# Kernel tuning notes

Measured on AMD Instinct MI355X. Metric: run time of the kernel, lower is better.

## Reference

```python
import jax, jax.numpy as jnp
import numpy as np

DIM = 384
HEADS = 6
HEAD_DIM = DIM // HEADS
MLP_DIM = int(DIM * 4.0)
EPS = 1e-5


def layer_norm(x, g, b):
    mu = jnp.mean(x, axis=-1, keepdims=True)
    var = jnp.mean(jnp.square(x - mu), axis=-1, keepdims=True)
    return (x - mu) * jax.lax.rsqrt(var + EPS) * g + b


def setup_inputs() -> dict:
    key = jax.random.key(0)
    ks = jax.random.split(key, 12)
    s = 0.02
    return {
        "x": jax.random.normal(ks[0], (8, 2048, DIM), dtype=jnp.float32),
        "ln1_g": jnp.ones((DIM,), jnp.float32),
        "ln1_b": jnp.zeros((DIM,), jnp.float32),
        "qkv_w": jax.random.normal(ks[1], (DIM, 3 * DIM), jnp.float32) * s,
        "qkv_b": jnp.zeros((3 * DIM,), jnp.float32),
        "proj_w": jax.random.normal(ks[2], (DIM, DIM), jnp.float32) * s,
        "proj_b": jnp.zeros((DIM,), jnp.float32),
        "ln2_g": jnp.ones((DIM,), jnp.float32),
        "ln2_b": jnp.zeros((DIM,), jnp.float32),
        "fc1_w": jax.random.normal(ks[3], (DIM, MLP_DIM), jnp.float32) * s,
        "fc1_b": jnp.zeros((MLP_DIM,), jnp.float32),
        "fc2_w": jax.random.normal(ks[4], (MLP_DIM, DIM), jnp.float32) * s,
        "fc2_b": jnp.zeros((DIM,), jnp.float32),
    }


def reference(x, ln1_g, ln1_b, qkv_w, qkv_b, proj_w, proj_b,
              ln2_g, ln2_b, fc1_w, fc1_b, fc2_w, fc2_b):
    B, N, C = x.shape
    # --- attention ---
    h = layer_norm(x, ln1_g, ln1_b)
    qkv = h @ qkv_w + qkv_b  # [B,N,3C]
    qkv = qkv.reshape(B, N, 3, HEADS, HEAD_DIM)
    q, k, v = jnp.moveaxis(qkv, 2, 0)  # each [B,N,H,D]
    scale = HEAD_DIM ** -0.5
    attn = jnp.einsum('bnhd,bmhd->bhnm', q, k) * scale  # [B,H,N,N]
    attn = jax.nn.softmax(attn, axis=-1)
    o = jnp.einsum('bhnm,bmhd->bnhd', attn, v).reshape(B, N, C)
    x = x + o @ proj_w + proj_b
    # --- mlp ---
    h = layer_norm(x, ln2_g, ln2_b)
    h = jax.nn.gelu(h @ fc1_w + fc1_b, approximate=False)
    x = x + h @ fc2_w + fc2_b
    return x
```

## Files before the change

kernel.cpp:

```cpp
#include <hip/hip_runtime.h>
#include <hip/hip_bf16.h>

#define DIM   384
#define SEQ   2048
#define BATCH 8
#define NHEAD 6
#define HD    64
#define MLPD  1536
#define MTOT  (BATCH*SEQ)

typedef __attribute__((ext_vector_type(8))) short bf16x8;
typedef __attribute__((ext_vector_type(4))) float f32x4;

static __device__ __forceinline__ float bf2f(unsigned short u){
    union { float f; unsigned int i; } v; v.i = ((unsigned int)u) << 16; return v.f;
}
static __device__ __forceinline__ unsigned short f2bf(float f){
    union { float f; unsigned int i; } v; v.f = f;
    unsigned int r = v.i + 0x7fffu + ((v.i >> 16) & 1u);
    return (unsigned short)(r >> 16);
}
static __device__ __forceinline__ unsigned int asu(float f){
    union { float f; unsigned int i; } v; v.f = f; return v.i;
}
static __device__ __forceinline__ void gload_lds16(const unsigned short* g, unsigned short* l){
    __builtin_amdgcn_global_load_lds(
        (__attribute__((address_space(1))) void*)(g),
        (__attribute__((address_space(3))) void*)(l), 16, 0, 0);
}
static __device__ __forceinline__ void barx(){
    asm volatile("" ::: "memory");
    __builtin_amdgcn_s_barrier();
    asm volatile("" ::: "memory");
}
#define WAITVM(N) asm volatile("s_waitcnt vmcnt(" #N ")" ::: "memory")

__global__ __launch_bounds__(256) void wt_all_kernel(
    const float* __restrict__ qkv_w, const float* __restrict__ proj_w,
    const float* __restrict__ fc1_w, const float* __restrict__ fc2_w,
    unsigned short* __restrict__ o_qkv, unsigned short* __restrict__ o_prj,
    unsigned short* __restrict__ o_fc1, unsigned short* __restrict__ o_fc2)
{
    __shared__ float tile[64][68];
    int bid = blockIdx.x;
    const float* W; unsigned short* Wt; int K, N, tk, tn;
    if (bid < 108)      { W = qkv_w; Wt = o_qkv; K = 384;  N = 1152; tk = bid/18;        tn = bid%18; }
    else if (bid < 144) { W = proj_w; Wt = o_prj; K = 384;  N = 384;  tk = (bid-108)/6;  tn = (bid-108)%6; }
    else if (bid < 288) { W = fc1_w; Wt = o_fc1; K = 384;  N = 1536; tk = (bid-144)/24; tn = (bid-144)%24; }
    else                { W = fc2_w; Wt = o_fc2; K = 1536; N = 384;  tk = (bid-288)/6;  tn = (bid-288)%6; }
    int t = threadIdx.x;
    int lr = t >> 4, lc = (t & 15) * 4;
#pragma unroll
    for (int p = 0; p < 4; p++){
        float4 v = *(const float4*)(W + (size_t)(tk*64 + p*16 + lr) * N + tn*64 + lc);
        *(float4*)&tile[p*16 + lr][lc] = v;
    }
    __syncthreads();
    int n = t >> 2, k0 = (t & 3) * 16;
    unsigned int w[8];
#pragma unroll
    for (int i = 0; i < 8; i++)
        w[i] = (unsigned int)f2bf(tile[k0 + 2*i][n]) | ((unsigned int)f2bf(tile[k0 + 2*i + 1][n]) << 16);
    unsigned short* dst = Wt + (size_t)(tn*64 + n) * K + tk*64 + k0;
    *(uint4*)(dst)     = make_uint4(w[0], w[1], w[2], w[3]);
    *(uint4*)(dst + 8) = make_uint4(w[4], w[5], w[6], w[7]);
}

__global__ __launch_bounds__(256) void ln_kernel(const float* __restrict__ x,
                                                 const float* __restrict__ g,
                                                 const float* __restrict__ b,
                                                 unsigned short* __restrict__ out){
    int row  = blockIdx.x * 4 + (threadIdx.x >> 6);
    int lane = threadIdx.x & 63;
    const float* xr = x + (size_t)row * DIM;
    float v[6];
#pragma unroll
    for (int p = 0; p < 3; p++){
        float2 t = *(const float2*)(xr + lane * 2 + p * 128);
        v[2*p] = t.x; v[2*p+1] = t.y;
    }
    float s = 0.f, sq = 0.f;
#pragma unroll
    for (int i = 0; i < 6; i++){ s += v[i]; sq += v[i] * v[i]; }
#pragma unroll
    for (int off = 1; off < 64; off <<= 1){
        s  += __shfl_xor(s, off);
        sq += __shfl_xor(sq, off);
    }
    float mu   = s * (1.0f / DIM);
    float var  = sq * (1.0f / DIM) - mu * mu;
    float rstd = rsqrtf(var + 1e-5f);
    unsigned short* orow = out + (size_t)row * DIM;
#pragma unroll
    for (int p = 0; p < 3; p++){
        int c = lane * 2 + p * 128;
        float h0 = (v[2*p]   - mu) * rstd * g[c]   + b[c];
        float h1 = (v[2*p+1] - mu) * rstd * g[c+1] + b[c+1];
        unsigned int pk = (unsigned int)f2bf(h0) | ((unsigned int)f2bf(h1) << 16);
        *(unsigned int*)(orow + c) = pk;
    }
}

template<int OFF>
static __device__ __forceinline__ void gemm_tile(const unsigned short* smem,
                                                 int wid, int quad, int l15,
                                                 f32x4 (&acc)[2][4])
{
#pragma unroll
    for (int kk = 0; kk < 2; kk++){
        bf16x8 af[2], bf[4];
#pragma unroll
        for (int i = 0; i < 2; i++){
            int r = wid*32 + i*16 + l15;
            af[i] = *(const bf16x8*)&smem[OFF + r * 64 + (((kk*4 + quad) ^ (l15 & 7)) * 8)];
        }
#pragma unroll
        for (int j = 0; j < 4; j++){
            int r = j*16 + l15;
            bf[j] = *(const bf16x8*)&smem[OFF + 8192 + r * 64 + (((kk*4 + quad) ^ (l15 & 7)) * 8)];
        }
#pragma unroll
        for (int i = 0; i < 2; i++)
#pragma unroll
            for (int j = 0; j < 4; j++)
                acc[i][j] = __builtin_amdgcn_mfma_f32_16x16x32_bf16(af[i], bf[j], acc[i][j], 0, 0, 0);
    }
}

template<int EPI, int K>
__global__ __launch_bounds__(256, 3) void gemm_kernel(
    const unsigned short* __restrict__ A, const unsigned short* __restrict__ Bt,
    const float* __restrict__ bias, int N,
    const float* __restrict__ resid, float* __restrict__ outf,
    unsigned short* __restrict__ outb,
    unsigned short* __restrict__ qb, unsigned short* __restrict__ kb2,
    unsigned short* __restrict__ vb)
{
    __shared__ __align__(16) unsigned short smem[2 * 12288];
    int t = threadIdx.x;
    int wid = t >> 6, lane = t & 63, quad = lane >> 4, l15 = lane & 15;
    int row0 = blockIdx.y * 128, col0 = blockIdx.x * 64;
    int sr = lane >> 3, sc = lane & 7;
    int scl = (sc ^ sr) * 8;

    const unsigned short* A0 = A  + (size_t)(row0 + wid*32 + sr) * K + scl;
    const unsigned short* B0 = Bt + (size_t)(col0 + wid*16 + sr) * K + scl;
    int kc = 0;

#define GSTAGE(LOFF) do { \
    _Pragma("unroll") \
    for (int jj = 0; jj < 4; jj++) \
        gload_lds16(A0 + jj*8*K + kc, &smem[(LOFF) + (wid*32 + jj*8) * 64]); \
    _Pragma("unroll") \
    for (int jj = 0; jj < 2; jj++) \
        gload_lds16(B0 + jj*8*K + kc, &smem[(LOFF) + 8192 + (wid*16 + jj*8) * 64]); \
    kc += 64; } while(0)

    f32x4 acc[2][4];
    f32x4 zz = {0.f, 0.f, 0.f, 0.f};
#pragma unroll
    for (int i = 0; i < 2; i++)
#pragma unroll
        for (int j = 0; j < 4; j++) acc[i][j] = zz;

    GSTAGE(0);
    constexpr int PAIRS = K / 128;
    for (int p = 0; p < PAIRS - 1; p++){
        GSTAGE(12288);
        WAITVM(6);
        barx();
        gemm_tile<0>(smem, wid, quad, l15, acc);
        barx();
        GSTAGE(0);
        WAITVM(6);
        barx();
        gemm_tile<12288>(smem, wid, quad, l15, acc);
        barx();
    }
    GSTAGE(12288);
    WAITVM(6);
    barx();
    gemm_tile<0>(smem, wid, quad, l15, acc);
    barx();
    WAITVM(0);
    barx();
    gemm_tile<12288>(smem, wid, quad, l15, acc);
#undef GSTAGE

    if (EPI == 0 && col0 >= 768){
        __syncthreads();
        unsigned short* T = smem;
#pragma unroll
        for (int i = 0; i < 2; i++)
#pragma unroll
            for (int j = 0; j < 4; j++){
                int gcl = j*16 + l15;
                float bia = bias[col0 + gcl];
                int nsl0 = wid*32 + i*16 + quad*4;
#pragma unroll
                for (int r = 0; r < 4; r++)
                    T[gcl * 136 + nsl0 + r] = f2bf(acc[i][j][r] + bia);
            }
        __syncthreads();
        int head = (col0 - 768) >> 6;
        int bidx = row0 >> 11, ns0 = row0 & 2047;
        int d = t >> 2, qq = t & 3;
        unsigned short* dst = vb + ((size_t)((bidx * NHEAD + head) * 64 + d)) * SEQ + ns0 + qq*32;
        const unsigned short* src = T + d * 136 + qq * 32;
#pragma unroll
        for (int m = 0; m < 4; m++)
            *(uint4*)(dst + m*8) = *(const uint4*)(src + m*8);
        return;
    }

    if (EPI == 0){
        int trip = (col0 >= 384) ? 1 : 0;
        int head = (col0 - trip*384) >> 6;
        unsigned short* dstp = trip ? kb2 : qb;
#pragma unroll
        for (int i = 0; i < 2; i++)
#pragma unroll
            for (int j = 0; j < 4; j++){
                int d = j*16 + l15;
                float bia = bias[col0 + d];
                int gr0 = row0 + wid*32 + i*16 + quad*4;
#pragma unroll
                for (int r = 0; r < 4; r++){
                    int gr = gr0 + r;
                    int bidx = gr >> 11, ns = gr & 2047;
                    dstp[((size_t)(bidx * NHEAD + head) * SEQ + ns) * 64 + d] =
                        f2bf(acc[i][j][r] + bia);
                }
            }
        return;
    }

#pragma unroll
    for (int i = 0; i < 2; i++){
#pragma unroll
        for (int j = 0; j < 4; j++){
            int gr0 = row0 + wid*32 + i*16 + quad*4;
            int gc  = col0 + j*16 + l15;
            float bia = bias[gc];
#pragma unroll
            for (int r = 0; r < 4; r++){
                int gr = gr0 + r;
                float val = acc[i][j][r] + bia;
                if (EPI == 1){
                    outf[(size_t)gr * N + gc] = resid[(size_t)gr * N + gc] + val;
                } else {
                    float u = val * (1.0f + 0.044715f * val * val);
                    float e = __builtin_amdgcn_exp2f(u * 2.3025851f);
                    outb[(size_t)gr * N + gc] = f2bf(val * e / (e + 1.0f));
                }
            }
        }
    }
}

template<int LOFF>
static __device__ __forceinline__ void attn_tile(
    const bf16x8 (&qf)[2][2], const bf16x8& ones,
    const unsigned short* const (&kf_ptr)[4][2],
    const unsigned short* const (&vf_ptr)[2][4],
    const unsigned short* const (&pf_ptr)[2][2],
    uint2* const (&pw_ptr)[2][4],
    f32x4 (&sacc)[2], f32x4 (&oacc)[2][4])
{
    const f32x4 zz = {0.f, 0.f, 0.f, 0.f};
    f32x4 st[2][4];
#pragma unroll
    for (int n = 0; n < 4; n++){
        bf16x8 kf0 = *(const bf16x8*)(kf_ptr[n][0] + LOFF);
        bf16x8 kf1 = *(const bf16x8*)(kf_ptr[n][1] + LOFF);
#pragma unroll
        for (int h = 0; h < 2; h++){
            f32x4 z = __builtin_amdgcn_mfma_f32_16x16x32_bf16(kf0, qf[h][0], zz, 0, 0, 0);
            st[h][n] = __builtin_amdgcn_mfma_f32_16x16x32_bf16(kf1, qf[h][1], z, 0, 0, 0);
        }
    }
#pragma unroll
    for (int h = 0; h < 2; h++){
#pragma unroll
        for (int n = 0; n < 4; n++){
            float p0 = __builtin_amdgcn_exp2f(st[h][n][0]);
            float p1 = __builtin_amdgcn_exp2f(st[h][n][1]);
            float p2 = __builtin_amdgcn_exp2f(st[h][n][2]);
            float p3 = __builtin_amdgcn_exp2f(st[h][n][3]);
            unsigned int w0 = __builtin_amdgcn_perm(asu(p1), asu(p0), 0x07060302u);
            unsigned int w1 = __builtin_amdgcn_perm(asu(p3), asu(p2), 0x07060302u);
            *pw_ptr[h][n] = make_uint2(w0, w1);
        }
    }
    asm volatile("s_waitcnt lgkmcnt(0)" ::: "memory");
#pragma unroll
    for (int c = 0; c < 2; c++){
        bf16x8 pf[2];
#pragma unroll
        for (int h = 0; h < 2; h++)
            pf[h] = *(const bf16x8*)pf_ptr[c][h];
        sacc[0] = __builtin_amdgcn_mfma_f32_16x16x32_bf16(ones, pf[0], sacc[0], 0, 0, 0);
        sacc[1] = __builtin_amdgcn_mfma_f32_16x16x32_bf16(ones, pf[1], sacc[1], 0, 0, 0);
#pragma unroll
        for (int dn = 0; dn < 4; dn++){
            bf16x8 vf = *(const bf16x8*)(vf_ptr[c][dn] + LOFF);
            oacc[0][dn] = __builtin_amdgcn_mfma_f32_16x16x32_bf16(vf, pf[0], oacc[0][dn], 0, 0, 0);
            oacc[1][dn] = __builtin_amdgcn_mfma_f32_16x16x32_bf16(vf, pf[1], oacc[1][dn], 0, 0, 0);
        }
    }
}

__global__ __launch_bounds__(256, 3) void attn_kernel(const unsigned short* __restrict__ Q,
                                                      const unsigned short* __restrict__ Kb,
                                                      const unsigned short* __restrict__ Vt,
                                                      unsigned short* __restrict__ O){
    __shared__ __align__(16) unsigned short smem[16384 + 4*2048];

    int bh = blockIdx.y, qt = blockIdx.x;
    int t = threadIdx.x, wid = t >> 6, lane = t & 63, quad = lane >> 4, l15 = lane & 15;
    int l7 = l15 & 7;
    int q0 = qt * 128 + wid * 32;
    const unsigned short* Qp = Q  + (size_t)bh * SEQ * 64;
    const unsigned short* Kp = Kb + (size_t)bh * SEQ * 64;
    const unsigned short* Vp = Vt + (size_t)bh * 64 * SEQ;
    int sr = lane >> 3, sc = lane & 7;
    int scl = (sc ^ sr) * 8;

    const float QSCALE = 0.125f * 1.44269504f;
    bf16x8 qf[2][2];
#pragma unroll
    for (int h = 0; h < 2; h++){
#pragma unroll
        for (int c = 0; c < 2; c++){
            union { uint4 u; unsigned short s[8]; } cv;
            cv.u = *(const uint4*)(Qp + (size_t)(q0 + h*16 + l15) * 64 + c * 32 + quad * 8);
            bf16x8 f;
#pragma unroll
            for (int j = 0; j < 8; j++) f[j] = (short)f2bf(bf2f(cv.s[j]) * QSCALE);
            qf[h][c] = f;
        }
    }

    bf16x8 ones;
#pragma unroll
    for (int j = 0; j < 8; j++) ones[j] = (short)0x3F80;

    f32x4 oacc[2][4], sacc[2];
    f32x4 zz = {0.f, 0.f, 0.f, 0.f};
#pragma unroll
    for (int h = 0; h < 2; h++){
        sacc[h] = zz;
#pragma unroll
        for (int dn = 0; dn < 4; dn++) oacc[h][dn] = zz;
    }
    unsigned short* P = &smem[16384 + wid * 2048];

    const unsigned short* kf_ptr[4][2];
#pragma unroll
    for (int n = 0; n < 4; n++){
        int kv = n * 16 + l15;
        kf_ptr[n][0] = &smem[kv * 64 + ((quad       ^ (kv & 7)) * 8)];
        kf_ptr[n][1] = &smem[kv * 64 + (((4 + quad) ^ (kv & 7)) * 8)];
    }
    const unsigned short* vf_ptr[2][4];
#pragma unroll
    for (int c = 0; c < 2; c++)
#pragma unroll
        for (int dn = 0; dn < 4; dn++){
            int d = dn * 16 + l15;
            vf_ptr[c][dn] = &smem[4096 + d * 64 + (((c*4 + quad) ^ (d & 7)) * 8)];
        }
    const unsigned short* pf_ptr[2][2];
#pragma unroll
    for (int c = 0; c < 2; c++)
#pragma unroll
        for (int h = 0; h < 2; h++)
            pf_ptr[c][h] = P + (h*16 + l15) * 64 + (((c*4 + quad) ^ l7) * 8);
    uint2* pw_ptr[2][4];
#pragma unroll
    for (int h = 0; h < 2; h++)
#pragma unroll
        for (int n = 0; n < 4; n++){
            int qloc = h * 16 + l15;
            int chunk = n * 2 + (quad >> 1);
            pw_ptr[h][n] = (uint2*)(P + qloc * 64 + ((chunk ^ l7) * 8) + (quad & 1) * 4);
        }
    const unsigned short* kstage[2];
    const unsigned short* vstage[2];
    unsigned short* klds[2];
    unsigned short* vlds[2];
#pragma unroll
    for (int jj = 0; jj < 2; jj++){
        int rb = wid * 16 + jj * 8;
        kstage[jj] = Kp + (size_t)(rb + sr) * 64 + scl;
        vstage[jj] = Vp + (size_t)(rb + sr) * SEQ + scl;
        klds[jj] = &smem[rb * 64];
        vlds[jj] = &smem[4096 + rb * 64];
    }

#define AISSUE(BOFF) do { \
    _Pragma("unroll") \
    for (int jj = 0; jj < 2; jj++){ \
        gload_lds16(kstage[jj], klds[jj] + (BOFF)); \
        gload_lds16(vstage[jj], vlds[jj] + (BOFF)); \
        kstage[jj] += 64 * 64; \
        vstage[jj] += 64; \
    } } while(0)

    AISSUE(0);
    for (int p = 0; p < SEQ/128 - 1; p++){
        AISSUE(8192);
        WAITVM(4);
        barx();
        attn_tile<0>(qf, ones, kf_ptr, vf_ptr, pf_ptr, pw_ptr, sacc, oacc);
        barx();
        AISSUE(0);
        WAITVM(4);
        barx();
        attn_tile<8192>(qf, ones, kf_ptr, vf_ptr, pf_ptr, pw_ptr, sacc, oacc);
        barx();
    }
    AISSUE(8192);
    WAITVM(4);
    barx();
    attn_tile<0>(qf, ones, kf_ptr, vf_ptr, pf_ptr, pw_ptr, sacc, oacc);
    barx();
    WAITVM(0);
    barx();
    attn_tile<8192>(qf, ones, kf_ptr, vf_ptr, pf_ptr, pw_ptr, sacc, oacc);
#undef AISSUE

    int b = bh / NHEAD, hh = bh - b * NHEAD;
#pragma unroll
    for (int h = 0; h < 2; h++){
        float rd = 1.0f / sacc[h][0];
        size_t row = (size_t)(b * SEQ + q0 + h*16 + l15);
#pragma unroll
        for (int dn = 0; dn < 4; dn++){
            float v0 = oacc[h][dn][0] * rd, v1 = oacc[h][dn][1] * rd;
            float v2 = oacc[h][dn][2] * rd, v3 = oacc[h][dn][3] * rd;
            unsigned int w0 = (unsigned int)f2bf(v0) | ((unsigned int)f2bf(v1) << 16);
            unsigned int w1 = (unsigned int)f2bf(v2) | ((unsigned int)f2bf(v3) << 16);
            *(uint2*)(O + row * DIM + hh * 64 + dn * 16 + quad * 4) = make_uint2(w0, w1);
        }
    }
}

extern "C" void kernel_launch(void* const* d_in, const int* in_sizes, int n_in,
                              void* d_out, int out_size, void* d_ws, size_t ws_size,
                              hipStream_t stream){
    const float* x      = (const float*)d_in[0];
    const float* ln1_g  = (const float*)d_in[1];
    const float* ln1_b  = (const float*)d_in[2];
    const float* qkv_w  = (const float*)d_in[3];
    const float* qkv_b  = (const float*)d_in[4];
    const float* proj_w = (const float*)d_in[5];
    const float* proj_b = (const float*)d_in[6];
    const float* ln2_g  = (const float*)d_in[7];
    const float* ln2_b  = (const float*)d_in[8];
    const float* fc1_w  = (const float*)d_in[9];
    const float* fc1_b  = (const float*)d_in[10];
    const float* fc2_w  = (const float*)d_in[11];
    const float* fc2_b  = (const float*)d_in[12];
    float* out = (float*)d_out;

    char* p = (char*)d_ws;
    auto take = [&](size_t n){ char* r = p; p += (n + 255) & ~(size_t)255; return r; };
    unsigned short* wt_qkv = (unsigned short*)take((size_t)1152 * 384 * 2);
    unsigned short* wt_prj = (unsigned short*)take((size_t)384 * 384 * 2);
    unsigned short* wt_fc1 = (unsigned short*)take((size_t)1536 * 384 * 2);
    unsigned short* wt_fc2 = (unsigned short*)take((size_t)384 * 1536 * 2);
    unsigned short* rbig   = (unsigned short*)take((size_t)MTOT * 4 * DIM * 2);
    unsigned short* h2     = (unsigned short*)take((size_t)MTOT * DIM * 2);
    float*          x1     = (float*)take((size_t)MTOT * DIM * 4);

    unsigned short* h1     = rbig;
    unsigned short* qb     = rbig + (size_t)MTOT * DIM;
    unsigned short* kb     = qb   + (size_t)MTOT * DIM;
    unsigned short* vb     = kb   + (size_t)MTOT * DIM;
    unsigned short* attn_o = rbig;
    unsigned short* hm     = rbig;

    wt_all_kernel<<<dim3(432), 256, 0, stream>>>(qkv_w, proj_w, fc1_w, fc2_w,
                                                 wt_qkv, wt_prj, wt_fc1, wt_fc2);
    ln_kernel<<<dim3(MTOT/4), 256, 0, stream>>>(x, ln1_g, ln1_b, h1);
    gemm_kernel<0,384><<<dim3(18, 128), 256, 0, stream>>>(h1, wt_qkv, qkv_b, 1152,
                                                     nullptr, nullptr, nullptr, qb, kb, vb);
    attn_kernel<<<dim3(SEQ/128, BATCH*NHEAD), 256, 0, stream>>>(qb, kb, vb, attn_o);
    gemm_kernel<1,384><<<dim3(6, 128), 256, 0, stream>>>(attn_o, wt_prj, proj_b, 384,
                                                     x, x1, nullptr, nullptr, nullptr, nullptr);
    ln_kernel<<<dim3(MTOT/4), 256, 0, stream>>>(x1, ln2_g, ln2_b, h2);
    gemm_kernel<2,384><<<dim3(24, 128), 256, 0, stream>>>(h2, wt_fc1, fc1_b, 1536,
                                                      nullptr, nullptr, hm, nullptr, nullptr, nullptr);
    gemm_kernel<1,1536><<<dim3(6, 128), 256, 0, stream>>>(hm, wt_fc2, fc2_b, 384,
                                                     x1, out, nullptr, nullptr, nullptr, nullptr);
}
```

Before: 305.4 us.

## Reshape GEMM tiles to 64x128 with 2x2 waves, XCD-aware block remap, MFMA priority

The GEMM block tile changes from 128x64 to 64x128, with waves arranged 2x2 instead of 4x1. The grid becomes 1D and is remapped so consecutive logical tiles land on the same XCD, which should improve L2 reuse of shared A/B panels. The V-transpose and Q/K scatter epilogues are rewritten for the new tile shape. The attention kernel gets the same XCD remap and raises wave priority around its MFMA sections. The remap assumes each grid size is divisible by 8, and the changed tile shape alters how much A versus B is reloaded.

New measurement: 268.3 us. -12.2%, faster.

```diff
diff --git a/kernel.cpp b/kernel.cpp
--- a/kernel.cpp
+++ b/kernel.cpp
@@ -34,6 +34,10 @@
     asm volatile("" ::: "memory");
 }
 #define WAITVM(N) asm volatile("s_waitcnt vmcnt(" #N ")" ::: "memory")
+
+static __device__ __forceinline__ int xcd_lin(){
+    return (blockIdx.x & 7) * ((int)gridDim.x >> 3) + ((int)blockIdx.x >> 3);
+}
 
 __global__ __launch_bounds__(256) void wt_all_kernel(
     const float* __restrict__ qkv_w, const float* __restrict__ proj_w,
@@ -103,7 +107,7 @@
 
 template<int OFF>
 static __device__ __forceinline__ void gemm_tile(const unsigned short* smem,
-                                                 int wid, int quad, int l15,
+                                                 int wm, int wn, int quad, int l15,
                                                  f32x4 (&acc)[2][4])
 {
 #pragma unroll
@@ -111,13 +115,13 @@
         bf16x8 af[2], bf[4];
 #pragma unroll
         for (int i = 0; i < 2; i++){
-            int r = wid*32 + i*16 + l15;
+            int r = wm*32 + i*16 + l15;
             af[i] = *(const bf16x8*)&smem[OFF + r * 64 + (((kk*4 + quad) ^ (l15 & 7)) * 8)];
         }
 #pragma unroll
         for (int j = 0; j < 4; j++){
-            int r = j*16 + l15;
-            bf[j] = *(const bf16x8*)&smem[OFF + 8192 + r * 64 + (((kk*4 + quad) ^ (l15 & 7)) * 8)];
+            int r = wn*64 + j*16 + l15;
+            bf[j] = *(const bf16x8*)&smem[OFF + 4096 + r * 64 + (((kk*4 + quad) ^ (l15 & 7)) * 8)];
         }
 #pragma unroll
         for (int i = 0; i < 2; i++)
@@ -127,7 +131,7 @@
     }
 }
 
-template<int EPI, int K>
+template<int EPI, int NC, int K>
 __global__ __launch_bounds__(256, 3) void gemm_kernel(
     const unsigned short* __restrict__ A, const unsigned short* __restrict__ Bt,
     const float* __restrict__ bias, int N,
@@ -139,21 +143,37 @@
     __shared__ __align__(16) unsigned short smem[2 * 12288];
     int t = threadIdx.x;
     int wid = t >> 6, lane = t & 63, quad = lane >> 4, l15 = lane & 15;
-    int row0 = blockIdx.y * 128, col0 = blockIdx.x * 64;
+    int wm = wid >> 1, wn = wid & 1;
+    int lin = xcd_lin();
+    int row0 = (lin / NC) * 64, col0 = (lin % NC) * 128;
     int sr = lane >> 3, sc = lane & 7;
     int scl = (sc ^ sr) * 8;
 
-    const unsigned short* A0 = A  + (size_t)(row0 + wid*32 + sr) * K + scl;
-    const unsigned short* B0 = Bt + (size_t)(col0 + wid*16 + sr) * K + scl;
+    const unsigned short* astage[2];
+    const unsigned short* bstage[4];
+    unsigned short* alds[2];
+    unsigned short* blds[4];
+#pragma unroll
+    for (int jj = 0; jj < 2; jj++){
+        int rb = wid * 16 + jj * 8;
+        astage[jj] = A + (size_t)(row0 + rb + sr) * K + scl;
+        alds[jj]   = (unsigned short*)&smem[rb * 64];
+    }
+#pragma unroll
+    for (int jj = 0; jj < 4; jj++){
+        int rb = wid * 32 + jj * 8;
+        bstage[jj] = Bt + (size_t)(col0 + rb + sr) * K + scl;
+        blds[jj]   = (unsigned short*)&smem[4096 + rb * 64];
+    }
     int kc = 0;
 
 #define GSTAGE(LOFF) do { \
     _Pragma("unroll") \
+    for (int jj = 0; jj < 2; jj++) \
+        gload_lds16(astage[jj] + kc, alds[jj] + (LOFF)); \
+    _Pragma("unroll") \
     for (int jj = 0; jj < 4; jj++) \
-        gload_lds16(A0 + jj*8*K + kc, &smem[(LOFF) + (wid*32 + jj*8) * 64]); \
-    _Pragma("unroll") \
-    for (int jj = 0; jj < 2; jj++) \
-        gload_lds16(B0 + jj*8*K + kc, &smem[(LOFF) + 8192 + (wid*16 + jj*8) * 64]); \
+        gload_lds16(bstage[jj] + kc, blds[jj] + (LOFF)); \
     kc += 64; } while(0)
 
     f32x4 acc[2][4];
@@ -169,22 +189,22 @@
         GSTAGE(12288);
         WAITVM(6);
         barx();
-        gemm_tile<0>(smem, wid, quad, l15, acc);
+        gemm_tile<0>(smem, wm, wn, quad, l15, acc);
         barx();
         GSTAGE(0);
         WAITVM(6);
         barx();
-        gemm_tile<12288>(smem, wid, quad, l15, acc);
+        gemm_tile<12288>(smem, wm, wn, quad, l15, acc);
         barx();
     }
     GSTAGE(12288);
     WAITVM(6);
     barx();
-    gemm_tile<0>(smem, wid, quad, l15, acc);
+    gemm_tile<0>(smem, wm, wn, quad, l15, acc);
     barx();
     WAITVM(0);
     barx();
-    gemm_tile<12288>(smem, wid, quad, l15, acc);
+    gemm_tile<12288>(smem, wm, wn, quad, l15, acc);
 #undef GSTAGE
 
     if (EPI == 0 && col0 >= 768){
@@ -194,53 +214,32 @@
         for (int i = 0; i < 2; i++)
 #pragma unroll
             for (int j = 0; j < 4; j++){
-                int gcl = j*16 + l15;
+                int gcl = wn*64 + j*16 + l15;
                 float bia = bias[col0 + gcl];
-                int nsl0 = wid*32 + i*16 + quad*4;
+                int nsl0 = wm*32 + i*16 + quad*4;
 #pragma unroll
                 for (int r = 0; r < 4; r++)
-                    T[gcl * 136 + nsl0 + r] = f2bf(acc[i][j][r] + bia);
+                    T[gcl * 72 + nsl0 + r] = f2bf(acc[i][j][r] + bia);
             }
         __syncthreads();
-        int head = (col0 - 768) >> 6;
+        int gc = t >> 1, half = t & 1;
+        int rem = (col0 - 768) + gc;
+        int head = rem >> 6, d = rem & 63;
         int bidx = row0 >> 11, ns0 = row0 & 2047;
-        int d = t >> 2, qq = t & 3;
-        unsigned short* dst = vb + ((size_t)((bidx * NHEAD + head) * 64 + d)) * SEQ + ns0 + qq*32;
-        const unsigned short* src = T + d * 136 + qq * 32;
+        unsigned short* dst = vb + ((size_t)((bidx * NHEAD + head) * 64 + d)) * SEQ + ns0 + half*32;
+        const unsigned short* src = T + gc * 72 + half*32;
 #pragma unroll
         for (int m = 0; m < 4; m++)
             *(uint4*)(dst + m*8) = *(const uint4*)(src + m*8);
         return;
     }
 
-    if (EPI == 0){
-        int trip = (col0 >= 384) ? 1 : 0;
-        int head = (col0 - trip*384) >> 6;
-        unsigned short* dstp = trip ? kb2 : qb;
-#pragma unroll
-        for (int i = 0; i < 2; i++)
-#pragma unroll
-            for (int j = 0; j < 4; j++){
-                int d = j*16 + l15;
-                float bia = bias[col0 + d];
-                int gr0 = row0 + wid*32 + i*16 + quad*4;
-#pragma unroll
-                for (int r = 0; r < 4; r++){
-                    int gr = gr0 + r;
-                    int bidx = gr >> 11, ns = gr & 2047;
-                    dstp[((size_t)(bidx * NHEAD + head) * SEQ + ns) * 64 + d] =
-                        f2bf(acc[i][j][r] + bia);
-                }
-            }
-        return;
-    }
-
 #pragma unroll
     for (int i = 0; i < 2; i++){
 #pragma unroll
         for (int j = 0; j < 4; j++){
-            int gr0 = row0 + wid*32 + i*16 + quad*4;
-            int gc  = col0 + j*16 + l15;
+            int gr0 = row0 + wm*32 + i*16 + quad*4;
+            int gc  = col0 + wn*64 + j*16 + l15;
             float bia = bias[gc];
 #pragma unroll
             for (int r = 0; r < 4; r++){
@@ -248,10 +247,17 @@
                 float val = acc[i][j][r] + bia;
                 if (EPI == 1){
                     outf[(size_t)gr * N + gc] = resid[(size_t)gr * N + gc] + val;
-                } else {
+                } else if (EPI == 2){
                     float u = val * (1.0f + 0.044715f * val * val);
                     float e = __builtin_amdgcn_exp2f(u * 2.3025851f);
                     outb[(size_t)gr * N + gc] = f2bf(val * e / (e + 1.0f));
+                } else {
+                    int trip = gc / 384, remq = gc - trip * 384;
+                    int head = remq >> 6, d = remq & 63;
+                    int bidx = gr >> 11, ns = gr & 2047;
+                    size_t off = ((size_t)(bidx * NHEAD + head) * SEQ + ns) * 64 + d;
+                    unsigned short* dstp = (trip == 0) ? qb : kb2;
+                    dstp[off] = f2bf(val);
                 }
             }
         }
@@ -269,6 +275,7 @@
 {
     const f32x4 zz = {0.f, 0.f, 0.f, 0.f};
     f32x4 st[2][4];
+    __builtin_amdgcn_s_setprio(1);
 #pragma unroll
     for (int n = 0; n < 4; n++){
         bf16x8 kf0 = *(const bf16x8*)(kf_ptr[n][0] + LOFF);
@@ -279,6 +286,7 @@
             st[h][n] = __builtin_amdgcn_mfma_f32_16x16x32_bf16(kf1, qf[h][1], z, 0, 0, 0);
         }
     }
+    __builtin_amdgcn_s_setprio(0);
 #pragma unroll
     for (int h = 0; h < 2; h++){
 #pragma unroll
@@ -293,6 +301,7 @@
         }
     }
     asm volatile("s_waitcnt lgkmcnt(0)" ::: "memory");
+    __builtin_amdgcn_s_setprio(1);
 #pragma unroll
     for (int c = 0; c < 2; c++){
         bf16x8 pf[2];
@@ -308,6 +317,7 @@
             oacc[1][dn] = __builtin_amdgcn_mfma_f32_16x16x32_bf16(vf, pf[1], oacc[1][dn], 0, 0, 0);
         }
     }
+    __builtin_amdgcn_s_setprio(0);
 }
 
 __global__ __launch_bounds__(256, 3) void attn_kernel(const unsigned short* __restrict__ Q,
@@ -316,7 +326,8 @@
                                                       unsigned short* __restrict__ O){
     __shared__ __align__(16) unsigned short smem[16384 + 4*2048];
 
-    int bh = blockIdx.y, qt = blockIdx.x;
+    int lin = xcd_lin();
+    int qt = lin & 15, bh = lin >> 4;
     int t = threadIdx.x, wid = t >> 6, lane = t & 63, quad = lane >> 4, l15 = lane & 15;
     int l7 = l15 & 7;
     int q0 = qt * 128 + wid * 32;
@@ -484,14 +495,14 @@
     wt_all_kernel<<<dim3(432), 256, 0, stream>>>(qkv_w, proj_w, fc1_w, fc2_w,
                                                  wt_qkv, wt_prj, wt_fc1, wt_fc2);
     ln_kernel<<<dim3(MTOT/4), 256, 0, stream>>>(x, ln1_g, ln1_b, h1);
-    gemm_kernel<0,384><<<dim3(18, 128), 256, 0, stream>>>(h1, wt_qkv, qkv_b, 1152,
+    gemm_kernel<0,9,384><<<dim3(2304), 256, 0, stream>>>(h1, wt_qkv, qkv_b, 1152,
                                                      nullptr, nullptr, nullptr, qb, kb, vb);
-    attn_kernel<<<dim3(SEQ/128, BATCH*NHEAD), 256, 0, stream>>>(qb, kb, vb, attn_o);
-    gemm_kernel<1,384><<<dim3(6, 128), 256, 0, stream>>>(attn_o, wt_prj, proj_b, 384,
-                                                     x, x1, nullptr, nullptr, nullptr, nullptr);
+    attn_kernel<<<dim3(768), 256, 0, stream>>>(qb, kb, vb, attn_o);
+    gemm_kernel<1,3,384><<<dim3(768), 256, 0, stream>>>(attn_o, wt_prj, proj_b, 384,
+                                                    x, x1, nullptr, nullptr, nullptr, nullptr);
     ln_kernel<<<dim3(MTOT/4), 256, 0, stream>>>(x1, ln2_g, ln2_b, h2);
-    gemm_kernel<2,384><<<dim3(24, 128), 256, 0, stream>>>(h2, wt_fc1, fc1_b, 1536,
+    gemm_kernel<2,12,384><<<dim3(3072), 256, 0, stream>>>(h2, wt_fc1, fc1_b, 1536,
                                                       nullptr, nullptr, hm, nullptr, nullptr, nullptr);
-    gemm_kernel<1,1536><<<dim3(6, 128), 256, 0, stream>>>(hm, wt_fc2, fc2_b, 384,
-                                                     x1, out, nullptr, nullptr, nullptr, nullptr);
-}
+    gemm_kernel<1,3,1536><<<dim3(768), 256, 0, stream>>>(hm, wt_fc2, fc2_b, 384,
+                                                    x1, out, nullptr, nullptr, nullptr, nullptr);
+}
```
